# Optimization experiments

Measured on AMD Instinct MI355X. Metric: run time of the kernel, lower is better.

## Reference

```python
import jax, jax.numpy as jnp
import numpy as np

N, F_NODE, F_FLOW, H, E, B, L = 131072, 64, 16, 128, 2097152, 256, 32


def setup_inputs() -> dict:
    key = jax.random.key(0)
    ks = jax.random.split(key, 24)
    gn = lambda k, s, sc: jax.random.normal(k, s, jnp.float32) * sc
    s_in = 1.0 / np.sqrt(F_NODE)
    s_h = 1.0 / np.sqrt(H)
    s_f = 1.0 / np.sqrt(F_FLOW)
    s_c = 1.0 / np.sqrt(2 * H + H // 2)
    inp = {
        "x": gn(ks[0], (N, F_NODE), 1.0),
        "edge_index": jax.random.randint(ks[1], (2, E), 0, N),
        "batch": jnp.sort(jax.random.randint(ks[2], (N,), 0, B)),
        "path_idx": jax.random.randint(ks[3], (B, L), 0, N),
        "path_len": jax.random.randint(ks[4], (B,), 1, L + 1),
        "flow": gn(ks[5], (B, F_FLOW), 1.0),
        # SAGEConv1: out = mean_agg(x_j) @ Wl.T + b + x_i @ Wr.T
        "Wl1": gn(ks[6], (H, F_NODE), s_in), "Wr1": gn(ks[7], (H, F_NODE), s_in), "b1": gn(ks[8], (H,), s_in),
        "Wl2": gn(ks[9], (H, H), s_h), "Wr2": gn(ks[10], (H, H), s_h), "b2": gn(ks[11], (H,), s_h),
        # LSTM (torch gate order i,f,g,o)
        "Wih": gn(ks[12], (4 * H, H), s_h), "Whh": gn(ks[13], (4 * H, H), s_h),
        "bih": gn(ks[14], (4 * H,), s_h), "bhh": gn(ks[15], (4 * H,), s_h),
        # flow encoder Linear(F_FLOW, H//2)
        "Wf": gn(ks[16], (H // 2, F_FLOW), s_f), "bf": gn(ks[17], (H // 2,), s_f),
        # scorer MLP: Linear(2H+H//2, H) -> ReLU -> Linear(H, 1)
        "Ws1": gn(ks[18], (H, 2 * H + H // 2), s_c), "bs1": gn(ks[19], (H,), s_c),
        "Ws2": gn(ks[20], (1, H), s_h), "bs2": gn(ks[21], (1,), s_h),
    }
    return inp


def _sage(x, src, dst, Wl, Wr, b, n):
    agg = jax.ops.segment_sum(x[src], dst, num_segments=n)  # [n, d]
    cnt = jax.ops.segment_sum(jnp.ones((src.shape[0],), x.dtype), dst, num_segments=n)
    mean = agg / jnp.maximum(cnt, 1.0)[:, None]
    return mean @ Wl.T + b + x @ Wr.T


def _lstm_final_h(seq, valid, Wih, Whh, bih, bhh):
    # seq: [B, L, H], valid: [B, L] bool; returns h at each path's last valid step
    b, l, h = seq.shape
    h0 = jnp.zeros((b, h), seq.dtype)

    def step(carry, inp):
        hp, cp = carry
        x_t, v = inp  # [B,H], [B]
        gates = x_t @ Wih.T + hp @ Whh.T + bih + bhh
        i, f, g, o = jnp.split(gates, 4, axis=-1)
        c_new = jax.nn.sigmoid(f) * cp + jax.nn.sigmoid(i) * jnp.tanh(g)
        h_new = jax.nn.sigmoid(o) * jnp.tanh(c_new)
        m = v[:, None]
        return (jnp.where(m, h_new, hp), jnp.where(m, c_new, cp)), None

    (hf, _), _ = jax.lax.scan(step, (h0, h0),
                              (jnp.swapaxes(seq, 0, 1), jnp.swapaxes(valid, 0, 1)))
    return hf


def reference(x, edge_index, batch, path_idx, path_len, flow,
              Wl1, Wr1, b1, Wl2, Wr2, b2,
              Wih, Whh, bih, bhh, Wf, bf, Ws1, bs1, Ws2, bs2):
    n = x.shape[0]
    src, dst = edge_index[0], edge_index[1]
    h1 = jax.nn.relu(_sage(x, src, dst, Wl1, Wr1, b1, n))
    node_emb = jax.nn.relu(_sage(h1, src, dst, Wl2, Wr2, b2, n))

    # global mean pool per graph
    gsum = jax.ops.segment_sum(node_emb, batch, num_segments=B)
    gcnt = jax.ops.segment_sum(jnp.ones((n,), node_emb.dtype), batch, num_segments=B)
    graph_emb = gsum / jnp.maximum(gcnt, 1.0)[:, None]  # [B, H]

    flow_emb = jax.nn.relu(flow @ Wf.T + bf)  # [B, H//2]

    path_seq = node_emb[path_idx]  # [B, L, H]
    valid = jnp.arange(L)[None, :] < path_len[:, None]  # [B, L]
    path_emb = _lstm_final_h(path_seq, valid, Wih, Whh, bih, bhh)  # [B, H]

    combined = jnp.concatenate([graph_emb, path_emb, flow_emb], axis=-1)
    hidden = jax.nn.relu(combined @ Ws1.T + bs1)
    scores = hidden @ Ws2.T + bs2  # [B, 1]
    return scores[:, 0]  # matches torch.cat of per-path [1] outputs -> [B]
```

## Files before the change

kernel.cpp:

```cpp
#include <hip/hip_runtime.h>
#include <hip/hip_bf16.h>

#define N_NODES 131072
#define N_EDGES 2097152
#define BATCHES 256
#define LPATH   32
#define NB   256
#define NPB  512
#define GB   256
#define EPB  8192

typedef __hip_bfloat16 bf16;
using short8  = __attribute__((ext_vector_type(8))) short;
using floatx4 = __attribute__((ext_vector_type(4))) float;

__device__ __forceinline__ float bl(unsigned u){ union {unsigned x; float f;} c; c.x = u << 16; return c.f; }
__device__ __forceinline__ float bh(unsigned u){ union {unsigned x; float f;} c; c.x = u & 0xffff0000u; return c.f; }
__device__ __forceinline__ unsigned packbf(float lo, float hi){
  bf16 l = __float2bfloat16(lo), h = __float2bfloat16(hi);
  unsigned short lu, hu;
  __builtin_memcpy(&lu, &l, 2); __builtin_memcpy(&hu, &h, 2);
  return (unsigned)lu | ((unsigned)hu << 16);
}
__device__ __forceinline__ float sigf(float x){ return 1.f / (1.f + __expf(-x)); }

__global__ void prep_k(const float* __restrict__ Wl1, const float* __restrict__ Wr1,
                       const float* __restrict__ Wl2, const float* __restrict__ Wr2,
                       const float* __restrict__ Wih, const float* __restrict__ Whh,
                       const float* __restrict__ bih, const float* __restrict__ bhh,
                       bf16* __restrict__ Wcat1, bf16* __restrict__ Wcat2,
                       bf16* __restrict__ WihB, bf16* __restrict__ WhhB, float* __restrict__ bsumF){
  int g = blockIdx.x * 256 + threadIdx.x;
  if (g < 16384) {
    int h = g >> 7, k = g & 127;
    float v = (k < 64) ? Wl1[h * 64 + k] : Wr1[h * 64 + (k - 64)];
    Wcat1[g] = __float2bfloat16(v);
  } else if (g < 49152) {
    int q = g - 16384;
    int h = q >> 8, k = q & 255;
    float v = (k < 128) ? Wl2[h * 128 + k] : Wr2[h * 128 + (k - 128)];
    Wcat2[q] = __float2bfloat16(v);
  } else if (g < 114688) {
    int q = g - 49152;
    WihB[q] = __float2bfloat16(Wih[q]);
  } else if (g < 180224) {
    int q = g - 114688;
    WhhB[q] = __float2bfloat16(Whh[q]);
  } else if (g < 180736) {
    int k = g - 180224;
    bsumF[k] = bih[k] + bhh[k];
  }
}

__global__ void xb16_k(const float* __restrict__ x, bf16* __restrict__ xb, bf16* __restrict__ Acat1){
  int g = blockIdx.x * 256 + threadIdx.x;
  int n = g >> 5, p = g & 31;
  float2 v = *(const float2*)(x + (size_t)n * 64 + p * 2);
  unsigned u = packbf(v.x, v.y);
  *(unsigned*)(xb + (size_t)n * 64 + p * 2) = u;
  *(unsigned*)(Acat1 + (size_t)n * 128 + 64 + p * 2) = u;
}

__global__ void bounds_k(const int* __restrict__ batch, int* __restrict__ starts){
  int b = threadIdx.x;
  int lo = 0, hi = N_NODES;
  while (lo < hi){ int mid = (lo + hi) >> 1; if (batch[mid] < b) lo = mid + 1; else hi = mid; }
  starts[b] = lo;
  if (b == 0) starts[BATCHES] = N_NODES;
}

__global__ void cntA_k(const int* __restrict__ dst, int* __restrict__ cntA){
  __shared__ int h[NB];
  int tid = threadIdx.x;
  h[tid] = 0;
  __syncthreads();
  int base = blockIdx.x * EPB;
  #pragma unroll
  for (int i = 0; i < EPB / 256; ++i){
    int d = dst[base + i * 256 + tid];
    atomicAdd(&h[d >> 9], 1);
  }
  __syncthreads();
  cntA[tid * GB + blockIdx.x] = h[tid];
}

__global__ void scan1_k(const int* __restrict__ cnt, int* __restrict__ ofsA, int* __restrict__ bsum){
  __shared__ int sh[256];
  int t = threadIdx.x, i = blockIdx.x * 256 + t;
  int v = cnt[i];
  sh[t] = v; __syncthreads();
  int inc = v;
  for (int d = 1; d < 256; d <<= 1){
    int add = (t >= d) ? sh[t - d] : 0;
    __syncthreads();
    inc += add; sh[t] = inc;
    __syncthreads();
  }
  ofsA[i] = inc - v;
  if (t == 255) bsum[blockIdx.x] = inc;
}

__global__ void scan2_k(const int* __restrict__ bsum, int* __restrict__ bsumEx){
  __shared__ int sh[NB];
  int t = threadIdx.x;
  int v = bsum[t];
  sh[t] = v; __syncthreads();
  int inc = v;
  for (int d = 1; d < NB; d <<= 1){
    int add = (t >= d) ? sh[t - d] : 0;
    __syncthreads();
    inc += add; sh[t] = inc;
    __syncthreads();
  }
  bsumEx[t] = inc - v;
}

__global__ void passA2_k(const int* __restrict__ src, const int* __restrict__ dst,
                         const int* __restrict__ ofsA, const int* __restrict__ bsumEx,
                         unsigned* __restrict__ ebuf){
  __shared__ int cur[NB];
  int tid = threadIdx.x;
  cur[tid] = ofsA[tid * GB + blockIdx.x] + bsumEx[tid];
  __syncthreads();
  int base = blockIdx.x * EPB;
  #pragma unroll
  for (int i = 0; i < EPB / 256; ++i){
    int e = base + i * 256 + tid;
    int s = src[e], d = dst[e];
    int p = atomicAdd(&cur[d >> 9], 1);
    ebuf[p] = (unsigned)s | ((unsigned)(d & (NPB - 1)) << 17);
  }
}

__global__ void passB_k(const unsigned* __restrict__ ebuf, const int* __restrict__ bsumEx,
                        int* __restrict__ offs, int* __restrict__ srcS){
  __shared__ int ncnt[NPB];
  __shared__ int pairs[256];
  __shared__ int nofs[NPB];
  int k = blockIdx.x, tid = threadIdx.x;
  int bs = bsumEx[k];
  int be = (k < NB - 1) ? bsumEx[k + 1] : N_EDGES;
  ncnt[tid] = 0; ncnt[tid + 256] = 0;
  __syncthreads();
  for (int i = bs + tid; i < be; i += 256)
    atomicAdd(&ncnt[ebuf[i] >> 17], 1);
  __syncthreads();
  int p = ncnt[2 * tid] + ncnt[2 * tid + 1];
  pairs[tid] = p;
  __syncthreads();
  int inc = p;
  for (int d = 1; d < 256; d <<= 1){
    int add = (tid >= d) ? pairs[tid - d] : 0;
    __syncthreads();
    inc += add; pairs[tid] = inc;
    __syncthreads();
  }
  int ex = inc - p;
  nofs[2 * tid]     = ex;
  nofs[2 * tid + 1] = ex + ncnt[2 * tid];
  __syncthreads();
  offs[k * NPB + tid]       = bs + nofs[tid];
  offs[k * NPB + tid + 256] = bs + nofs[tid + 256];
  if (k == NB - 1 && tid == 0) offs[N_NODES] = N_EDGES;
  ncnt[tid] = nofs[tid]; ncnt[tid + 256] = nofs[tid + 256];
  __syncthreads();
  for (int i = bs + tid; i < be; i += 256){
    unsigned w = ebuf[i];
    int loc = w >> 17, sv = w & 0x1FFFF;
    int pp = atomicAdd(&ncnt[loc], 1);
    srcS[bs + pp] = sv;
  }
}

__global__ void agg1_k(const bf16* __restrict__ xb, const int* __restrict__ offs,
                       const int* __restrict__ srcS, bf16* __restrict__ Acat1){
  int wid = threadIdx.x >> 6, lane = threadIdx.x & 63;
  int n = blockIdx.x * 4 + wid;
  int s = offs[n], e = offs[n + 1];
  int slot = lane >> 3, fl = lane & 7;
  float a0=0,a1=0,a2=0,a3=0,a4=0,a5=0,a6=0,a7=0;
  float c0=0,c1=0,c2=0,c3=0,c4=0,c5=0,c6=0,c7=0;
  int i = s + slot;
  for (; i + 8 < e; i += 16){
    int sv0 = srcS[i], sv1 = srcS[i + 8];
    uint4 u = *(const uint4*)(xb + (size_t)sv0 * 64 + fl * 8);
    uint4 v = *(const uint4*)(xb + (size_t)sv1 * 64 + fl * 8);
    a0 += bl(u.x); a1 += bh(u.x); a2 += bl(u.y); a3 += bh(u.y);
    a4 += bl(u.z); a5 += bh(u.z); a6 += bl(u.w); a7 += bh(u.w);
    c0 += bl(v.x); c1 += bh(v.x); c2 += bl(v.y); c3 += bh(v.y);
    c4 += bl(v.z); c5 += bh(v.z); c6 += bl(v.w); c7 += bh(v.w);
  }
  if (i < e){
    int sv0 = srcS[i];
    uint4 u = *(const uint4*)(xb + (size_t)sv0 * 64 + fl * 8);
    a0 += bl(u.x); a1 += bh(u.x); a2 += bl(u.y); a3 += bh(u.y);
    a4 += bl(u.z); a5 += bh(u.z); a6 += bl(u.w); a7 += bh(u.w);
  }
  a0 += c0; a1 += c1; a2 += c2; a3 += c3;
  a4 += c4; a5 += c5; a6 += c6; a7 += c7;
  a0 += __shfl_xor(a0, 8); a0 += __shfl_xor(a0, 16); a0 += __shfl_xor(a0, 32);
  a1 += __shfl_xor(a1, 8); a1 += __shfl_xor(a1, 16); a1 += __shfl_xor(a1, 32);
  a2 += __shfl_xor(a2, 8); a2 += __shfl_xor(a2, 16); a2 += __shfl_xor(a2, 32);
  a3 += __shfl_xor(a3, 8); a3 += __shfl_xor(a3, 16); a3 += __shfl_xor(a3, 32);
  a4 += __shfl_xor(a4, 8); a4 += __shfl_xor(a4, 16); a4 += __shfl_xor(a4, 32);
  a5 += __shfl_xor(a5, 8); a5 += __shfl_xor(a5, 16); a5 += __shfl_xor(a5, 32);
  a6 += __shfl_xor(a6, 8); a6 += __shfl_xor(a6, 16); a6 += __shfl_xor(a6, 32);
  a7 += __shfl_xor(a7, 8); a7 += __shfl_xor(a7, 16); a7 += __shfl_xor(a7, 32);
  if (slot == 0){
    int d = e - s; if (d < 1) d = 1;
    float inv = 1.f / (float)d;
    uint4 w;
    w.x = packbf(a0 * inv, a1 * inv); w.y = packbf(a2 * inv, a3 * inv);
    w.z = packbf(a4 * inv, a5 * inv); w.w = packbf(a6 * inv, a7 * inv);
    *(uint4*)(Acat1 + (size_t)n * 128 + fl * 8) = w;
  }
}

__global__ void agg2_k(const int* __restrict__ offs, const int* __restrict__ srcS, bf16* __restrict__ Acat2){
  int wid = threadIdx.x >> 6, lane = threadIdx.x & 63;
  int n = blockIdx.x * 4 + wid;
  int s = offs[n], e = offs[n + 1];
  int slot = lane >> 4, fl = lane & 15;
  float a0=0,a1=0,a2=0,a3=0,a4=0,a5=0,a6=0,a7=0;
  float c0=0,c1=0,c2=0,c3=0,c4=0,c5=0,c6=0,c7=0;
  int i = s + slot;
  for (; i + 4 < e; i += 8){
    int sv0 = srcS[i], sv1 = srcS[i + 4];
    uint4 u = *(const uint4*)(Acat2 + (size_t)sv0 * 256 + 128 + fl * 8);
    uint4 v = *(const uint4*)(Acat2 + (size_t)sv1 * 256 + 128 + fl * 8);
    a0 += bl(u.x); a1 += bh(u.x); a2 += bl(u.y); a3 += bh(u.y);
    a4 += bl(u.z); a5 += bh(u.z); a6 += bl(u.w); a7 += bh(u.w);
    c0 += bl(v.x); c1 += bh(v.x); c2 += bl(v.y); c3 += bh(v.y);
    c4 += bl(v.z); c5 += bh(v.z); c6 += bl(v.w); c7 += bh(v.w);
  }
  if (i < e){
    int sv0 = srcS[i];
    uint4 u = *(const uint4*)(Acat2 + (size_t)sv0 * 256 + 128 + fl * 8);
    a0 += bl(u.x); a1 += bh(u.x); a2 += bl(u.y); a3 += bh(u.y);
    a4 += bl(u.z); a5 += bh(u.z); a6 += bl(u.w); a7 += bh(u.w);
  }
  a0 += c0; a1 += c1; a2 += c2; a3 += c3;
  a4 += c4; a5 += c5; a6 += c6; a7 += c7;
  a0 += __shfl_xor(a0, 16); a0 += __shfl_xor(a0, 32);
  a1 += __shfl_xor(a1, 16); a1 += __shfl_xor(a1, 32);
  a2 += __shfl_xor(a2, 16); a2 += __shfl_xor(a2, 32);
  a3 += __shfl_xor(a3, 16); a3 += __shfl_xor(a3, 32);
  a4 += __shfl_xor(a4, 16); a4 += __shfl_xor(a4, 32);
  a5 += __shfl_xor(a5, 16); a5 += __shfl_xor(a5, 32);
  a6 += __shfl_xor(a6, 16); a6 += __shfl_xor(a6, 32);
  a7 += __shfl_xor(a7, 16); a7 += __shfl_xor(a7, 32);
  if (slot == 0){
    int d = e - s; if (d < 1) d = 1;
    float inv = 1.f / (float)d;
    uint4 w;
    w.x = packbf(a0 * inv, a1 * inv); w.y = packbf(a2 * inv, a3 * inv);
    w.z = packbf(a4 * inv, a5 * inv); w.w = packbf(a6 * inv, a7 * inv);
    *(uint4*)(Acat2 + (size_t)n * 256 + fl * 8) = w;
  }
}

__global__ __launch_bounds__(256) void gemm_k(const bf16* __restrict__ A, int lda,
                                              const bf16* __restrict__ W, int K,
                                              const float* __restrict__ bias,
                                              void* __restrict__ out, int ldo, int outF32, int relu){
  __shared__ bf16 Wl[128][136];
  int tid = threadIdx.x;
  int wid = tid >> 6, lane = tid & 63;
  int l16 = lane & 15, quad = lane >> 4;
  int rowBase  = blockIdx.x * 64 + wid * 16;
  int colGroup = blockIdx.y * 128;
  floatx4 acc[8] = {};
  int nStage = K >> 7;
  for (int ks = 0; ks < nStage; ++ks){
    __syncthreads();
    for (int c = tid; c < 2048; c += 256){
      int r = c >> 4, kc = (c & 15) << 3;
      *(uint4*)(&Wl[r][kc]) = *(const uint4*)(W + (size_t)(colGroup + r) * K + ks * 128 + kc);
    }
    __syncthreads();
    for (int kk = 0; kk < 4; ++kk){
      short8 af = *(const short8*)(A + (size_t)(rowBase + l16) * lda + ks * 128 + kk * 32 + quad * 8);
      #pragma unroll
      for (int c = 0; c < 8; ++c){
        short8 bq = *(const short8*)(&Wl[c * 16 + l16][kk * 32 + quad * 8]);
        acc[c] = __builtin_amdgcn_mfma_f32_16x16x32_bf16(af, bq, acc[c], 0, 0, 0);
      }
    }
  }
  #pragma unroll
  for (int c = 0; c < 8; ++c){
    int col = colGroup + c * 16 + l16;
    float bv = bias ? bias[col] : 0.f;
    #pragma unroll
    for (int r = 0; r < 4; ++r){
      int row = rowBase + quad * 4 + r;
      float v = acc[c][r] + bv;
      if (relu) v = fmaxf(v, 0.f);
      if (outF32) ((float*)out)[(size_t)row * ldo + col] = v;
      else        ((bf16*)out)[(size_t)row * ldo + col]  = __float2bfloat16(v);
    }
  }
}

__global__ void pool_k(const bf16* __restrict__ ne, const int* __restrict__ starts, float* __restrict__ comb){
  __shared__ float sh[8][128];
  int b = blockIdx.x;
  int q = threadIdx.x >> 6, lane = threadIdx.x & 63;
  int s = starts[b], e = starts[b + 1];
  float a0 = 0.f, a1 = 0.f;
  for (int i = s + q; i < e; i += 8){
    unsigned u = *(const unsigned*)(ne + (size_t)i * 128 + lane * 2);
    a0 += bl(u); a1 += bh(u);
  }
  sh[q][lane * 2] = a0; sh[q][lane * 2 + 1] = a1;
  __syncthreads();
  if (threadIdx.x < 128){
    int f = threadIdx.x;
    float tot = 0.f;
    #pragma unroll
    for (int k = 0; k < 8; ++k) tot += sh[k][f];
    int d = e - s; if (d < 1) d = 1;
    comb[b * 320 + f] = tot / (float)d;
  }
}

__global__ void flow_k(const float* __restrict__ flow, const float* __restrict__ Wf,
                       const float* __restrict__ bfv, float* __restrict__ comb){
  int g = blockIdx.x * 256 + threadIdx.x;
  int b = g >> 6, j = g & 63;
  float acc = bfv[j];
  for (int k = 0; k < 16; ++k)
    acc += flow[b * 16 + k] * Wf[j * 16 + k];
  comb[b * 320 + 256 + j] = fmaxf(acc, 0.f);
}

__global__ void gather_k(const int* __restrict__ path_idx, const bf16* __restrict__ ne, bf16* __restrict__ ps){
  int wid = threadIdx.x >> 6, lane = threadIdx.x & 63;
  int r = blockIdx.x * 4 + wid;
  int idx = path_idx[r];
  ((unsigned*)ps)[(size_t)r * 64 + lane] = ((const unsigned*)ne)[(size_t)idx * 64 + lane];
}

__global__ __launch_bounds__(256, 1) void lstm_k(const bf16* __restrict__ Whh, const float* __restrict__ pre,
                                                 const int* __restrict__ path_len, float* __restrict__ comb){
  __shared__ float h[128];
  __shared__ float g[512];
  int b = blockIdx.x, j = threadIdx.x;
  uint4 wa[16], wb[16];
  const uint4* w0 = (const uint4*)(Whh + (size_t)j * 128);
  const uint4* w1 = (const uint4*)(Whh + (size_t)(j + 256) * 128);
  #pragma unroll
  for (int k = 0; k < 16; ++k){ wa[k] = w0[k]; wb[k] = w1[k]; }
  if (j < 128) h[j] = 0.f;
  float c = 0.f, hn = 0.f;
  int len = path_len[b]; if (len < 1) len = 1; if (len > LPATH) len = LPATH;
  const float4* hv4 = (const float4*)h;
  for (int t = 0; t < len; ++t){
    __syncthreads();
    float a0 = pre[((size_t)b * LPATH + t) * 512 + j];
    float a1 = pre[((size_t)b * LPATH + t) * 512 + j + 256];
    #pragma unroll
    for (int k = 0; k < 16; ++k){
      float4 h0 = hv4[2 * k], h1 = hv4[2 * k + 1];
      uint4 u = wa[k], v = wb[k];
      a0 = fmaf(bl(u.x), h0.x, a0); a0 = fmaf(bh(u.x), h0.y, a0);
      a0 = fmaf(bl(u.y), h0.z, a0); a0 = fmaf(bh(u.y), h0.w, a0);
      a0 = fmaf(bl(u.z), h1.x, a0); a0 = fmaf(bh(u.z), h1.y, a0);
      a0 = fmaf(bl(u.w), h1.z, a0); a0 = fmaf(bh(u.w), h1.w, a0);
      a1 = fmaf(bl(v.x), h0.x, a1); a1 = fmaf(bh(v.x), h0.y, a1);
      a1 = fmaf(bl(v.y), h0.z, a1); a1 = fmaf(bh(v.y), h0.w, a1);
      a1 = fmaf(bl(v.z), h1.x, a1); a1 = fmaf(bh(v.z), h1.y, a1);
      a1 = fmaf(bl(v.w), h1.z, a1); a1 = fmaf(bh(v.w), h1.w, a1);
    }
    g[j] = a0; g[j + 256] = a1;
    __syncthreads();
    if (j < 128){
      float ig = sigf(g[j]), fg = sigf(g[j + 128]);
      float gg = tanhf(g[j + 256]), og = sigf(g[j + 384]);
      c = fg * c + ig * gg;
      hn = og * tanhf(c);
      h[j] = hn;
    }
  }
  if (j < 128) comb[b * 320 + 128 + j] = hn;
}

__global__ void head_k(const float* __restrict__ comb, const float* __restrict__ Ws1, const float* __restrict__ bs1,
                       const float* __restrict__ Ws2, const float* __restrict__ bs2, float* __restrict__ out){
  __shared__ float cl[320];
  __shared__ float red[128];
  int b = blockIdx.x, j = threadIdx.x;
  for (int k = j; k < 320; k += 128) cl[k] = comb[b * 320 + k];
  __syncthreads();
  float acc = bs1[j];
  const float4* wr = (const float4*)(Ws1 + (size_t)j * 320);
  #pragma unroll 4
  for (int kc = 0; kc < 80; ++kc){
    float4 u = wr[kc];
    int k = kc * 4;
    acc += u.x * cl[k] + u.y * cl[k + 1] + u.z * cl[k + 2] + u.w * cl[k + 3];
  }
  float hv = fmaxf(acc, 0.f);
  red[j] = hv * Ws2[j];
  __syncthreads();
  for (int s = 64; s > 0; s >>= 1){ if (j < s) red[j] += red[j + s]; __syncthreads(); }
  if (j == 0) out[b] = red[0] + bs2[0];
}

constexpr size_t OFF_OFFS   = 0;
constexpr size_t OFF_CNTA   = 524544;
constexpr size_t OFF_OFSA   = OFF_CNTA   + 262144;
constexpr size_t OFF_BSUM   = OFF_OFSA   + 262144;
constexpr size_t OFF_BSUMEX = OFF_BSUM   + 1024;
constexpr size_t OFF_STARTS = OFF_BSUMEX + 1024;
constexpr size_t OFF_SRCS   = OFF_STARTS + 2048;
constexpr size_t OFF_WCAT1  = OFF_SRCS   + 8388608;
constexpr size_t OFF_WCAT2  = OFF_WCAT1  + 32768;
constexpr size_t OFF_WIHB   = OFF_WCAT2  + 65536;
constexpr size_t OFF_WHHB   = OFF_WIHB   + 131072;
constexpr size_t OFF_BSUMF  = OFF_WHHB   + 131072;
constexpr size_t OFF_COMB   = OFF_BSUMF  + 2048;
constexpr size_t OFF_ACAT1  = OFF_COMB   + 327680;
constexpr size_t OFF_ACAT2  = OFF_ACAT1  + 33554432;
constexpr size_t OFF_EBUF   = OFF_ACAT2;
constexpr size_t OFF_PATHSEQ= OFF_ACAT2;
constexpr size_t OFF_PRE    = OFF_ACAT2  + 2097152;
constexpr size_t OFF_XB     = OFF_ACAT2  + 50331648;

extern "C" void kernel_launch(void* const* d_in, const int* in_sizes, int n_in,
                              void* d_out, int out_size, void* d_ws, size_t ws_size,
                              hipStream_t stream){
  const float* x      = (const float*)d_in[0];
  const int* edge     = (const int*)d_in[1];
  const int* batch    = (const int*)d_in[2];
  const int* path_idx = (const int*)d_in[3];
  const int* path_len = (const int*)d_in[4];
  const float* flow   = (const float*)d_in[5];
  const float* Wl1 = (const float*)d_in[6];
  const float* Wr1 = (const float*)d_in[7];
  const float* b1  = (const float*)d_in[8];
  const float* Wl2 = (const float*)d_in[9];
  const float* Wr2 = (const float*)d_in[10];
  const float* b2  = (const float*)d_in[11];
  const float* Wih = (const float*)d_in[12];
  const float* Whh = (const float*)d_in[13];
  const float* bih = (const float*)d_in[14];
  const float* bhh = (const float*)d_in[15];
  const float* Wf  = (const float*)d_in[16];
  const float* bfv = (const float*)d_in[17];
  const float* Ws1 = (const float*)d_in[18];
  const float* bs1 = (const float*)d_in[19];
  const float* Ws2 = (const float*)d_in[20];
  const float* bs2 = (const float*)d_in[21];

  char* ws = (char*)d_ws;
  int* offs    = (int*)(ws + OFF_OFFS);
  int* cntA    = (int*)(ws + OFF_CNTA);
  int* ofsA    = (int*)(ws + OFF_OFSA);
  int* bsum    = (int*)(ws + OFF_BSUM);
  int* bsumEx  = (int*)(ws + OFF_BSUMEX);
  int* starts  = (int*)(ws + OFF_STARTS);
  int* srcS    = (int*)(ws + OFF_SRCS);
  bf16* Wcat1  = (bf16*)(ws + OFF_WCAT1);
  bf16* Wcat2  = (bf16*)(ws + OFF_WCAT2);
  bf16* WihB   = (bf16*)(ws + OFF_WIHB);
  bf16* WhhB   = (bf16*)(ws + OFF_WHHB);
  float* bsumF = (float*)(ws + OFF_BSUMF);
  float* comb  = (float*)(ws + OFF_COMB);
  bf16* Acat1  = (bf16*)(ws + OFF_ACAT1);
  bf16* node_emb = Acat1;
  bf16* Acat2  = (bf16*)(ws + OFF_ACAT2);
  unsigned* ebuf = (unsigned*)(ws + OFF_EBUF);
  bf16* pathseq= (bf16*)(ws + OFF_PATHSEQ);
  float* pre   = (float*)(ws + OFF_PRE);
  bf16* xb     = (bf16*)(ws + OFF_XB);

  prep_k<<<707, 256, 0, stream>>>(Wl1, Wr1, Wl2, Wr2, Wih, Whh, bih, bhh, Wcat1, Wcat2, WihB, WhhB, bsumF);
  xb16_k<<<N_NODES / 8, 256, 0, stream>>>(x, xb, Acat1);
  bounds_k<<<1, 256, 0, stream>>>(batch, starts);
  cntA_k<<<GB, 256, 0, stream>>>(edge + N_EDGES, cntA);
  scan1_k<<<NB, 256, 0, stream>>>(cntA, ofsA, bsum);
  scan2_k<<<1, NB, 0, stream>>>(bsum, bsumEx);
  passA2_k<<<GB, 256, 0, stream>>>(edge, edge + N_EDGES, ofsA, bsumEx, ebuf);
  passB_k<<<NB, 256, 0, stream>>>(ebuf, bsumEx, offs, srcS);
  agg1_k<<<N_NODES / 4, 256, 0, stream>>>(xb, offs, srcS, Acat1);
  gemm_k<<<dim3(N_NODES / 64, 1), 256, 0, stream>>>(Acat1, 128, Wcat1, 128, b1, Acat2 + 128, 256, 0, 1);
  agg2_k<<<N_NODES / 4, 256, 0, stream>>>(offs, srcS, Acat2);
  gemm_k<<<dim3(N_NODES / 64, 1), 256, 0, stream>>>(Acat2, 256, Wcat2, 256, b2, node_emb, 128, 0, 1);
  pool_k<<<BATCHES, 512, 0, stream>>>(node_emb, starts, comb);
  flow_k<<<64, 256, 0, stream>>>(flow, Wf, bfv, comb);
  gather_k<<<BATCHES * LPATH / 4, 256, 0, stream>>>(path_idx, node_emb, pathseq);
  gemm_k<<<dim3(BATCHES * LPATH / 64, 4), 256, 0, stream>>>(pathseq, 128, WihB, 128, bsumF, pre, 512, 1, 0);
  lstm_k<<<BATCHES, 256, 0, stream>>>(WhhB, pre, path_len, comb);
  head_k<<<BATCHES, 128, 0, stream>>>(comb, Ws1, bs1, Ws2, bs2, (float*)d_out);
}
```

Before: 486.4 us.

## Batch 16 paths per block in LSTM and use MFMA for recurrent matmul

The LSTM kernel now handles 16 paths per block instead of one. Each step's recurrent h·Whh^T is computed with bf16 16x16x32 MFMA instructions, with Whh fragments held in registers and h double-buffered in shared memory as bf16. The next step's input pre-activations are prefetched, and sigmoid/tanh use a fast reciprocal-exp form. This is meant to cut the serial scalar-FMA latency of each step, at the cost of bf16 rounding of the hidden state, only 16 blocks in the grid, and every block iterating to the longest path among its 16.

Result: faster. 458.4 us (-5.8%).

```diff
diff --git a/kernel.cpp b/kernel.cpp
--- a/kernel.cpp
+++ b/kernel.cpp
@@ -22,7 +22,9 @@
   __builtin_memcpy(&lu, &l, 2); __builtin_memcpy(&hu, &h, 2);
   return (unsigned)lu | ((unsigned)hu << 16);
 }
-__device__ __forceinline__ float sigf(float x){ return 1.f / (1.f + __expf(-x)); }
+__device__ __forceinline__ float frcp(float x){ return __builtin_amdgcn_rcpf(x); }
+__device__ __forceinline__ float sigf(float x){ return frcp(1.f + __expf(-x)); }
+__device__ __forceinline__ float tanh_fast(float x){ return fmaf(2.f, frcp(1.f + __expf(-2.f * x)), -1.f); }
 
 __global__ void prep_k(const float* __restrict__ Wl1, const float* __restrict__ Wr1,
                        const float* __restrict__ Wl2, const float* __restrict__ Wr2,
@@ -343,46 +345,114 @@
 
 __global__ __launch_bounds__(256, 1) void lstm_k(const bf16* __restrict__ Whh, const float* __restrict__ pre,
                                                  const int* __restrict__ path_len, float* __restrict__ comb){
-  __shared__ float h[128];
-  __shared__ float g[512];
-  int b = blockIdx.x, j = threadIdx.x;
-  uint4 wa[16], wb[16];
-  const uint4* w0 = (const uint4*)(Whh + (size_t)j * 128);
-  const uint4* w1 = (const uint4*)(Whh + (size_t)(j + 256) * 128);
-  #pragma unroll
-  for (int k = 0; k < 16; ++k){ wa[k] = w0[k]; wb[k] = w1[k]; }
-  if (j < 128) h[j] = 0.f;
-  float c = 0.f, hn = 0.f;
-  int len = path_len[b]; if (len < 1) len = 1; if (len > LPATH) len = LPATH;
-  const float4* hv4 = (const float4*)h;
-  for (int t = 0; t < len; ++t){
-    __syncthreads();
-    float a0 = pre[((size_t)b * LPATH + t) * 512 + j];
-    float a1 = pre[((size_t)b * LPATH + t) * 512 + j + 256];
-    #pragma unroll
-    for (int k = 0; k < 16; ++k){
-      float4 h0 = hv4[2 * k], h1 = hv4[2 * k + 1];
-      uint4 u = wa[k], v = wb[k];
-      a0 = fmaf(bl(u.x), h0.x, a0); a0 = fmaf(bh(u.x), h0.y, a0);
-      a0 = fmaf(bl(u.y), h0.z, a0); a0 = fmaf(bh(u.y), h0.w, a0);
-      a0 = fmaf(bl(u.z), h1.x, a0); a0 = fmaf(bh(u.z), h1.y, a0);
-      a0 = fmaf(bl(u.w), h1.z, a0); a0 = fmaf(bh(u.w), h1.w, a0);
-      a1 = fmaf(bl(v.x), h0.x, a1); a1 = fmaf(bh(v.x), h0.y, a1);
-      a1 = fmaf(bl(v.y), h0.z, a1); a1 = fmaf(bh(v.y), h0.w, a1);
-      a1 = fmaf(bl(v.z), h1.x, a1); a1 = fmaf(bh(v.z), h1.y, a1);
-      a1 = fmaf(bl(v.w), h1.z, a1); a1 = fmaf(bh(v.w), h1.w, a1);
+  __shared__ bf16 hbuf[2][16][136];
+  int tid = threadIdx.x;
+  int w = tid >> 6, lane = tid & 63;
+  int l16 = lane & 15, quad = lane >> 4;
+  int b0 = blockIdx.x * 16;
+
+  short8 wb[4][2][4];
+  #pragma unroll
+  for (int q = 0; q < 4; ++q)
+    #pragma unroll
+    for (int hf = 0; hf < 2; ++hf){
+      const bf16* rp = Whh + (size_t)(q * 128 + w * 32 + hf * 16 + l16) * 128 + quad * 8;
+      #pragma unroll
+      for (int ks = 0; ks < 4; ++ks) wb[q][hf][ks] = *(const short8*)(rp + ks * 32);
     }
-    g[j] = a0; g[j + 256] = a1;
-    __syncthreads();
-    if (j < 128){
-      float ig = sigf(g[j]), fg = sigf(g[j + 128]);
-      float gg = tanhf(g[j + 256]), og = sigf(g[j + 384]);
-      c = fg * c + ig * gg;
-      hn = og * tanhf(c);
-      h[j] = hn;
-    }
-  }
-  if (j < 128) comb[b * 320 + 128 + j] = hn;
+
+  int lenr[4];
+  #pragma unroll
+  for (int r = 0; r < 4; ++r){
+    int L = path_len[b0 + quad * 4 + r];
+    if (L < 1) L = 1; if (L > LPATH) L = LPATH;
+    lenr[r] = L;
+  }
+  int maxlen = 1;
+  for (int i = 0; i < 16; ++i){
+    int L = path_len[b0 + i];
+    if (L > LPATH) L = LPATH;
+    if (L > maxlen) maxlen = L;
+  }
+
+  for (int i = tid; i < 1088; i += 256) ((unsigned*)&hbuf[0][0][0])[i] = 0;
+
+  const float* pb[4];
+  #pragma unroll
+  for (int r = 0; r < 4; ++r)
+    pb[r] = pre + (size_t)(b0 + quad * 4 + r) * LPATH * 512 + w * 32 + l16;
+
+  float pv[4][2][4];
+  #pragma unroll
+  for (int q = 0; q < 4; ++q)
+    #pragma unroll
+    for (int hf = 0; hf < 2; ++hf)
+      #pragma unroll
+      for (int r = 0; r < 4; ++r)
+        pv[q][hf][r] = pb[r][q * 128 + hf * 16];
+
+  float cst[2][4] = {}, hst[2][4] = {};
+
+  for (int t = 0; t < maxlen; ++t){
+    int cur = t & 1, nxt = cur ^ 1;
+    __syncthreads();
+    short8 af[4];
+    #pragma unroll
+    for (int ks = 0; ks < 4; ++ks)
+      af[ks] = *(const short8*)(&hbuf[cur][l16][ks * 32 + quad * 8]);
+    int tn = (t + 1 < maxlen) ? t + 1 : t;
+    float pnext[4][2][4];
+    #pragma unroll
+    for (int q = 0; q < 4; ++q)
+      #pragma unroll
+      for (int hf = 0; hf < 2; ++hf)
+        #pragma unroll
+        for (int r = 0; r < 4; ++r)
+          pnext[q][hf][r] = pb[r][tn * 512 + q * 128 + hf * 16];
+    floatx4 acc[4][2];
+    #pragma unroll
+    for (int q = 0; q < 4; ++q)
+      #pragma unroll
+      for (int hf = 0; hf < 2; ++hf){
+        acc[q][hf][0] = pv[q][hf][0]; acc[q][hf][1] = pv[q][hf][1];
+        acc[q][hf][2] = pv[q][hf][2]; acc[q][hf][3] = pv[q][hf][3];
+      }
+    #pragma unroll
+    for (int ks = 0; ks < 4; ++ks)
+      #pragma unroll
+      for (int q = 0; q < 4; ++q)
+        #pragma unroll
+        for (int hf = 0; hf < 2; ++hf)
+          acc[q][hf] = __builtin_amdgcn_mfma_f32_16x16x32_bf16(af[ks], wb[q][hf][ks], acc[q][hf], 0, 0, 0);
+    #pragma unroll
+    for (int hf = 0; hf < 2; ++hf)
+      #pragma unroll
+      for (int r = 0; r < 4; ++r){
+        float ig = sigf(acc[0][hf][r]);
+        float fg = sigf(acc[1][hf][r]);
+        float gg = tanh_fast(acc[2][hf][r]);
+        float og = sigf(acc[3][hf][r]);
+        float cn = fmaf(fg, cst[hf][r], ig * gg);
+        float hn = og * tanh_fast(cn);
+        bool vld = t < lenr[r];
+        cst[hf][r] = vld ? cn : cst[hf][r];
+        hst[hf][r] = vld ? hn : hst[hf][r];
+        hbuf[nxt][quad * 4 + r][w * 32 + hf * 16 + l16] = __float2bfloat16(hst[hf][r]);
+      }
+    #pragma unroll
+    for (int q = 0; q < 4; ++q)
+      #pragma unroll
+      for (int hf = 0; hf < 2; ++hf)
+        #pragma unroll
+        for (int r = 0; r < 4; ++r)
+          pv[q][hf][r] = pnext[q][hf][r];
+  }
+
+  #pragma unroll
+  for (int hf = 0; hf < 2; ++hf)
+    #pragma unroll
+    for (int r = 0; r < 4; ++r)
+      comb[(b0 + quad * 4 + r) * 320 + 128 + w * 32 + hf * 16 + l16] = hst[hf][r];
 }
 
 __global__ void head_k(const float* __restrict__ comb, const float* __restrict__ Ws1, const float* __restrict__ bs1,
@@ -491,6 +561,6 @@
   flow_k<<<64, 256, 0, stream>>>(flow, Wf, bfv, comb);
   gather_k<<<BATCHES * LPATH / 4, 256, 0, stream>>>(path_idx, node_emb, pathseq);
   gemm_k<<<dim3(BATCHES * LPATH / 64, 4), 256, 0, stream>>>(pathseq, 128, WihB, 128, bsumF, pre, 512, 1, 0);
-  lstm_k<<<BATCHES, 256, 0, stream>>>(WhhB, pre, path_len, comb);
+  lstm_k<<<BATCHES / 16, 256, 0, stream>>>(WhhB, pre, path_len, comb);
   head_k<<<BATCHES, 128, 0, stream>>>(comb, Ws1, bs1, Ws2, bs2, (float*)d_out);
 }
```
